# Kernel tuning notes

Measured on AMD Instinct MI355X. Metric: run time of the kernel, lower is better.

The kernel has to match this reference:

```python
import jax, jax.numpy as jnp
import numpy as np


def setup_inputs() -> dict:
    key = jax.random.key(0)
    k1, k2 = jax.random.split(key)
    B, S_ENC, S_DEC, D = 8, 2048, 2048, 1024
    enc_outputs = jax.random.normal(k1, (B, S_ENC, D), dtype=jnp.float32)
    dec_outputs = jax.random.normal(k2, (B, S_DEC, D), dtype=jnp.float32)
    return {"enc_outputs": enc_outputs, "dec_outputs": dec_outputs}


def reference(enc_outputs, dec_outputs):
    # scores: [B, S_enc, S_dec] = enc @ dec^T (unscaled)
    a_t = jnp.einsum('bed,btd->bet', enc_outputs, dec_outputs)
    a_t = jax.nn.softmax(a_t, axis=-1)
    # context: [B, S_dec, D] = a_t^T @ enc
    c_t = jnp.einsum('bet,bed->btd', a_t, enc_outputs)
    return c_t
```

## Files before the change

kernel.cpp:

```cpp
#include <hip/hip_runtime.h>


typedef _Float16 half8 __attribute__((ext_vector_type(8)));
typedef _Float16 half4v __attribute__((ext_vector_type(4)));
typedef float floatx4 __attribute__((ext_vector_type(4)));

__device__ __forceinline__ void async_load16(const _Float16* g, void* l) {
  __builtin_amdgcn_global_load_lds(
      (const __attribute__((address_space(1))) void*)g,
      (__attribute__((address_space(3))) void*)l, 16, 0, 0);
}

template <typename OutT, bool STATS>
__global__ __launch_bounds__(512, 2) void gemm8p(
    const _Float16* __restrict__ A, const _Float16* __restrict__ Bt,
    OutT* __restrict__ C, float2* __restrict__ part_out, int K, long strideA,
    long strideB, long strideC, int ldA, int ldB, int ldC) {
  extern __shared__ char smem_[];
  const int tid = threadIdx.x;
  const int lane = tid & 63;
  const int wave = tid >> 6;
  const int wm = wave >> 2;
  const int wn = wave & 3;
  const int l15 = lane & 15;
  const int lh = lane >> 4;

  const int gx = gridDim.x, gxy = gridDim.x * gridDim.y;
  int fid = blockIdx.z * gxy + blockIdx.y * gx + blockIdx.x;
  const int nwg = gxy * gridDim.z;
  fid = (fid & 7) * (nwg >> 3) + (fid >> 3);
  const int b = fid / gxy;
  const int rem = fid - b * gxy;
  const int m0 = (rem / gx) * 256;
  const int n0 = (rem % gx) * 256;

  A += (long)b * strideA + (long)m0 * ldA;
  Bt += (long)b * strideB + (long)n0 * ldB;
  C += (long)b * strideC;

  const int lb0 = l15 * 128 + ((lh ^ (l15 & 7)) << 4);
  const int lb1 = lb0 ^ 64;
  const char* aBuf[2] = {smem_ + wm * 16384, smem_ + 32768 + wm * 16384};
  const char* bBuf[2] = {
      smem_ + 65536 + (wn >> 1) * 16384 + (wn & 1) * 8192,
      smem_ + 98304 + (wn >> 1) * 16384 + (wn & 1) * 8192};
  char* aSlot[2] = {smem_, smem_ + 32768};
  char* bSlot[2] = {smem_ + 65536, smem_ + 98304};

  const int srow = tid >> 3;
  const int skk = ((tid & 7) ^ (srow & 7)) << 3;
  const _Float16* Ast = A + (long)srow * ldA + skk;
  const _Float16* Bst = Bt + (long)srow * ldB + skk;
  const int dst = tid << 4;

  floatx4 acc[8][4] = {};
  half8 a[4][2], b0[2][2], b1[2][2];

  auto stage = [&](const _Float16* gs, int ld, int k0, char* slot) {
#pragma unroll
    for (int i = 0; i < 4; ++i)
      async_load16(gs + (long)(i * 64) * ld + k0, slot + i * 8192 + dst);
  };
  auto mm = [&](int mh, int nh, half8(&bb)[2][2]) {
    __builtin_amdgcn_s_setprio(1);
#pragma unroll
    for (int s = 0; s < 2; ++s)
#pragma unroll
      for (int q = 0; q < 4; ++q)
#pragma unroll
        for (int n = 0; n < 2; ++n)
          acc[mh * 4 + q][nh * 2 + n] = __builtin_amdgcn_mfma_f32_16x16x32_f16(
              a[q][s], bb[n][s], acc[mh * 4 + q][nh * 2 + n], 0, 0, 0);
    __builtin_amdgcn_s_setprio(0);
  };
  auto bar = [&]() { asm volatile("s_barrier" ::: "memory"); };

  auto quad4 = [&](int cur, int kst, bool last) {
    const char* aB_ = aBuf[cur];
    const char* bB_ = bBuf[cur];
#pragma unroll
    for (int q = 0; q < 4; ++q) {
      a[q][0] = *(const half8*)(aB_ + lb0 + q * 2048);
      a[q][1] = *(const half8*)(aB_ + lb1 + q * 2048);
    }
#pragma unroll
    for (int n = 0; n < 2; ++n) {
      b0[n][0] = *(const half8*)(bB_ + lb0 + n * 2048);
      b0[n][1] = *(const half8*)(bB_ + lb1 + n * 2048);
      b1[n][0] = *(const half8*)(bB_ + lb0 + (n + 2) * 2048);
      b1[n][1] = *(const half8*)(bB_ + lb1 + (n + 2) * 2048);
    }
    bar();
    mm(0, 0, b0);
    bar();
    bar();
    mm(0, 1, b1);
    bar();
#pragma unroll
    for (int q = 0; q < 4; ++q) {
      a[q][0] = *(const half8*)(aB_ + lb0 + (q + 4) * 2048);
      a[q][1] = *(const half8*)(aB_ + lb1 + (q + 4) * 2048);
    }
    if (kst >= 0) stage(Bst, ldB, kst, bSlot[cur]);
    bar();
    mm(1, 1, b1);
    bar();
    if (kst >= 0) stage(Ast, ldA, kst, aSlot[cur]);
    mm(1, 0, b0);
    if (last)
      asm volatile("s_waitcnt vmcnt(0)" ::: "memory");
    else
      asm volatile("s_waitcnt vmcnt(8)" ::: "memory");
    bar();
  };

  stage(Ast, ldA, 0, aSlot[0]);
  stage(Bst, ldB, 0, bSlot[0]);
  stage(Ast, ldA, 64, aSlot[1]);
  stage(Bst, ldB, 64, bSlot[1]);
  asm volatile("s_waitcnt vmcnt(8)" ::: "memory");
  bar();

  const int NT = K >> 6;
  for (int i = 0; i < (NT >> 1) - 1; ++i) {
    quad4(0, (2 * i + 2) * 64, false);
    quad4(1, (2 * i + 3) * 64, false);
  }
  quad4(0, -1, true);
  quad4(1, -1, true);

#pragma unroll
  for (int mf = 0; mf < 8; ++mf) {
    const long r0 = (long)(m0 + wm * 128 + mf * 16 + lh * 4);
#pragma unroll
    for (int nf = 0; nf < 4; ++nf) {
      const int cc = n0 + wn * 64 + nf * 16 + l15;
#pragma unroll
      for (int rr = 0; rr < 4; ++rr)
        C[(r0 + rr) * ldC + cc] = (OutT)acc[mf][nf][rr];
    }
  }

  if constexpr (STATS) {
    float2* sm = (float2*)smem_;
#pragma unroll
    for (int nf = 0; nf < 4; ++nf) {
      float x16[8][4];
#pragma unroll
      for (int mf = 0; mf < 8; ++mf)
#pragma unroll
        for (int rr = 0; rr < 4; ++rr)
          x16[mf][rr] = (float)(_Float16)acc[mf][nf][rr];
      float mx = -1e30f;
#pragma unroll
      for (int mf = 0; mf < 8; ++mf)
#pragma unroll
        for (int rr = 0; rr < 4; ++rr) mx = fmaxf(mx, x16[mf][rr]);
      float ss = 0.f;
#pragma unroll
      for (int mf = 0; mf < 8; ++mf)
#pragma unroll
        for (int rr = 0; rr < 4; ++rr) ss += __expf(x16[mf][rr] - mx);
#pragma unroll
      for (int d = 16; d <= 32; d <<= 1) {
        const float om = __shfl_xor(mx, d, 64);
        const float os = __shfl_xor(ss, d, 64);
        const float m2 = fmaxf(mx, om);
        ss = ss * __expf(mx - m2) + os * __expf(om - m2);
        mx = m2;
      }
      if (lh == 0) sm[wm * 256 + wn * 64 + nf * 16 + l15] = make_float2(mx, ss);
    }
    __syncthreads();
    if (tid < 256) {
      const float2 a0 = sm[tid], a1 = sm[256 + tid];
      const float m2 = fmaxf(a0.x, a1.x);
      const float s2 =
          a0.y * __expf(a0.x - m2) + a1.y * __expf(a1.x - m2);
      part_out[(size_t)(m0 >> 8) * 16384 + (size_t)b * 2048 + n0 + tid] =
          make_float2(m2, s2);
    }
  }
}

__global__ __launch_bounds__(256) void conv_enc(const float* __restrict__ E,
                                                _Float16* __restrict__ Eh,
                                                _Float16* __restrict__ EhT,
                                                int Se, int D) {
  __shared__ _Float16 T[64][72];
  const int b = blockIdx.z;
  const int d0 = blockIdx.x * 64;
  const int e0 = blockIdx.y * 64;
  const float* Eb = E + (size_t)b * Se * D;
  _Float16* Ehb = Eh + (size_t)b * Se * D;
  _Float16* EhTb = EhT + (size_t)b * D * Se;
  const int tid = threadIdx.x;
  const int tx = tid & 15;
  const int ty = tid >> 4;

  half4v h[4];
#pragma unroll
  for (int r = 0; r < 4; ++r) {
    const int e = e0 + ty * 4 + r;
    float4 v = *(const float4*)(Eb + (size_t)e * D + d0 + tx * 4);
    h[r][0] = (_Float16)v.x; h[r][1] = (_Float16)v.y;
    h[r][2] = (_Float16)v.z; h[r][3] = (_Float16)v.w;
    *(half4v*)(Ehb + (size_t)e * D + d0 + tx * 4) = h[r];
  }
#pragma unroll
  for (int c = 0; c < 4; ++c) {
    half4v w;
#pragma unroll
    for (int r = 0; r < 4; ++r) w[r] = h[r][c];
    *(half4v*)&T[tx * 4 + c][ty * 4] = w;
  }
  __syncthreads();
#pragma unroll
  for (int p = 0; p < 2; ++p) {
    const int idx = tid + p * 256;
    const int row = idx >> 3;
    const int ck = idx & 7;
    *(half8*)(EhTb + (size_t)(d0 + row) * Se + e0 + ck * 8) =
        *(const half8*)&T[row][ck * 8];
  }
}

__global__ __launch_bounds__(256) void conv_dec(const float* __restrict__ X,
                                                _Float16* __restrict__ Y) {
  const size_t i = ((size_t)blockIdx.x * 256 + threadIdx.x) * 8;
  float4 a = *(const float4*)(X + i);
  float4 b = *(const float4*)(X + i + 4);
  half8 h;
  h[0] = (_Float16)a.x; h[1] = (_Float16)a.y;
  h[2] = (_Float16)a.z; h[3] = (_Float16)a.w;
  h[4] = (_Float16)b.x; h[5] = (_Float16)b.y;
  h[6] = (_Float16)b.z; h[7] = (_Float16)b.w;
  *(half8*)(Y + i) = h;
}

__global__ __launch_bounds__(256) void stats_combine(
    const float2* __restrict__ part, float* __restrict__ cstat) {
  const int idx = blockIdx.x * 256 + threadIdx.x;
  float2 a = part[idx];
#pragma unroll
  for (int tc = 1; tc < 8; ++tc) {
    const float2 o = part[tc * 16384 + idx];
    const float m2 = fmaxf(a.x, o.x);
    a.y = a.y * __expf(a.x - m2) + o.y * __expf(o.x - m2);
    a.x = m2;
  }
  cstat[idx] = -(a.x * 1.44269504f + log2f(a.y));
}

__global__ __launch_bounds__(256) void norm_stream(
    const _Float16* __restrict__ ST, const float* __restrict__ cstat,
    _Float16* __restrict__ P) {
  const int b = blockIdx.y;
  const int t0 = blockIdx.x * 4;
  const int e = threadIdx.x * 8;
  float c_[8];
  *(float4*)c_ = *(const float4*)(cstat + (size_t)b * 2048 + e);
  *(float4*)(c_ + 4) = *(const float4*)(cstat + (size_t)b * 2048 + e + 4);
  const size_t base = ((size_t)b * 2048 + t0) * 2048 + e;
#pragma unroll
  for (int r = 0; r < 4; ++r) {
    half8 v = *(const half8*)(ST + base + (size_t)r * 2048);
    half8 o;
#pragma unroll
    for (int j = 0; j < 8; ++j)
      o[j] = (_Float16)exp2f((float)v[j] * 1.44269504f + c_[j]);
    *(half8*)(P + base + (size_t)r * 2048) = o;
  }
}

extern "C" void kernel_launch(void* const* d_in, const int* in_sizes, int n_in,
                              void* d_out, int out_size, void* d_ws,
                              size_t ws_size, hipStream_t stream) {
  const float* enc = (const float*)d_in[0];
  const float* dec = (const float*)d_in[1];
  float* out = (float*)d_out;

  const int B = 8, SE = 2048, SD = 2048, D = 1024;
  char* ws = (char*)d_ws;
  _Float16* enc_h = (_Float16*)ws;
  _Float16* dec_h = (_Float16*)(ws + 33554432);
  _Float16* P = (_Float16*)ws;
  _Float16* enc_hT = (_Float16*)(ws + 67108864);
  _Float16* ST = (_Float16*)(ws + 100663296);
  float* cstat = (float*)(ws + 167772160);
  float2* part2 = (float2*)(ws + 167903232);

  static int smem_set = 0;
  if (!smem_set) {
    (void)hipFuncSetAttribute(
        reinterpret_cast<const void*>(&gemm8p<_Float16, true>),
        hipFuncAttributeMaxDynamicSharedMemorySize, 131072);
    (void)hipFuncSetAttribute(
        reinterpret_cast<const void*>(&gemm8p<float, false>),
        hipFuncAttributeMaxDynamicSharedMemorySize, 131072);
    smem_set = 1;
  }

  conv_enc<<<dim3(D / 64, SE / 64, B), 256, 0, stream>>>(enc, enc_h, enc_hT,
                                                         SE, D);
  conv_dec<<<dim3((size_t)B * SD * D / 2048), 256, 0, stream>>>(dec, dec_h);
  gemm8p<_Float16, true><<<dim3(SE / 256, SD / 256, B), 512, 131072, stream>>>(
      dec_h, enc_h, ST, part2, D, (long)SD * D, (long)SE * D, (long)SD * SE,
      D, D, SE);
  stats_combine<<<dim3(64), 256, 0, stream>>>(part2, cstat);
  norm_stream<<<dim3(512, B), 256, 0, stream>>>(ST, cstat, P);
  gemm8p<float, false><<<dim3(D / 256, SD / 256, B), 512, 131072, stream>>>(
      P, enc_hT, out, nullptr, SE, (long)SD * SE, (long)D * SE, (long)SD * D,
      SE, SE, D);
}
```

Baseline: 321.0 us.

## Software-pipeline LDS fragment reads across k-tiles with double-buffered A registers

Restructures the GEMM main loop so the A and B fragments for the next k-tile are read from LDS during the last MFMA block of the current tile, using two A register sets that alternate between iterations. Each quad4 now starts its MFMAs immediately instead of stalling on LDS reads, and the barrier count per quad drops. The cost is higher VGPR pressure from the extra A buffer, which could spill or hurt occupancy under launch_bounds(512,2), and the wait/barrier ordering becomes more delicate.

```diff
diff --git a/kernel.cpp b/kernel.cpp
--- a/kernel.cpp
+++ b/kernel.cpp
@@ -54,14 +54,14 @@
   const int dst = tid << 4;
 
   floatx4 acc[8][4] = {};
-  half8 a[4][2], b0[2][2], b1[2][2];
+  half8 A0[4][2], A1[4][2], b0[2][2], b1[2][2];
 
   auto stage = [&](const _Float16* gs, int ld, int k0, char* slot) {
 #pragma unroll
     for (int i = 0; i < 4; ++i)
       async_load16(gs + (long)(i * 64) * ld + k0, slot + i * 8192 + dst);
   };
-  auto mm = [&](int mh, int nh, half8(&bb)[2][2]) {
+  auto mm = [&](int mh, int nh, half8(&aa)[4][2], half8(&bb)[2][2]) {
     __builtin_amdgcn_s_setprio(1);
 #pragma unroll
     for (int s = 0; s < 2; ++s)
@@ -70,47 +70,48 @@
 #pragma unroll
         for (int n = 0; n < 2; ++n)
           acc[mh * 4 + q][nh * 2 + n] = __builtin_amdgcn_mfma_f32_16x16x32_f16(
-              a[q][s], bb[n][s], acc[mh * 4 + q][nh * 2 + n], 0, 0, 0);
+              aa[q][s], bb[n][s], acc[mh * 4 + q][nh * 2 + n], 0, 0, 0);
     __builtin_amdgcn_s_setprio(0);
   };
   auto bar = [&]() { asm volatile("s_barrier" ::: "memory"); };
-
-  auto quad4 = [&](int cur, int kst, bool last) {
+  auto rdA = [&](half8(&d)[4][2], const char* base, int qo) {
+#pragma unroll
+    for (int q = 0; q < 4; ++q) {
+      d[q][0] = *(const half8*)(base + lb0 + (q + qo) * 2048);
+      d[q][1] = *(const half8*)(base + lb1 + (q + qo) * 2048);
+    }
+  };
+  auto rdB = [&](half8(&d)[2][2], const char* base, int no) {
+#pragma unroll
+    for (int n = 0; n < 2; ++n) {
+      d[n][0] = *(const half8*)(base + lb0 + (n + no) * 2048);
+      d[n][1] = *(const half8*)(base + lb1 + (n + no) * 2048);
+    }
+  };
+
+  auto quad4 = [&](int cur, int kst, bool pf, bool hs, half8(&aC)[4][2],
+                   half8(&aN)[4][2]) {
     const char* aB_ = aBuf[cur];
     const char* bB_ = bBuf[cur];
-#pragma unroll
-    for (int q = 0; q < 4; ++q) {
-      a[q][0] = *(const half8*)(aB_ + lb0 + q * 2048);
-      a[q][1] = *(const half8*)(aB_ + lb1 + q * 2048);
-    }
-#pragma unroll
-    for (int n = 0; n < 2; ++n) {
-      b0[n][0] = *(const half8*)(bB_ + lb0 + n * 2048);
-      b0[n][1] = *(const half8*)(bB_ + lb1 + n * 2048);
-      b1[n][0] = *(const half8*)(bB_ + lb0 + (n + 2) * 2048);
-      b1[n][1] = *(const half8*)(bB_ + lb1 + (n + 2) * 2048);
-    }
+    mm(0, 0, aC, b0);
+    rdB(b1, bB_, 2);
     bar();
-    mm(0, 0, b0);
+    mm(0, 1, aC, b1);
+    rdA(aC, aB_, 4);
+    if (hs) stage(Bst, ldB, kst, bSlot[cur]);
     bar();
+    mm(1, 1, aC, b1);
+    if (hs) stage(Ast, ldA, kst, aSlot[cur]);
+    if (pf) {
+      if (hs)
+        asm volatile("s_waitcnt vmcnt(8)" ::: "memory");
+      else
+        asm volatile("s_waitcnt vmcnt(0)" ::: "memory");
+    }
     bar();
-    mm(0, 1, b1);
-    bar();
-#pragma unroll
-    for (int q = 0; q < 4; ++q) {
-      a[q][0] = *(const half8*)(aB_ + lb0 + (q + 4) * 2048);
-      a[q][1] = *(const half8*)(aB_ + lb1 + (q + 4) * 2048);
-    }
-    if (kst >= 0) stage(Bst, ldB, kst, bSlot[cur]);
-    bar();
-    mm(1, 1, b1);
-    bar();
-    if (kst >= 0) stage(Ast, ldA, kst, aSlot[cur]);
-    mm(1, 0, b0);
-    if (last)
-      asm volatile("s_waitcnt vmcnt(0)" ::: "memory");
-    else
-      asm volatile("s_waitcnt vmcnt(8)" ::: "memory");
+    if (pf) rdA(aN, aBuf[cur ^ 1], 0);
+    mm(1, 0, aC, b0);
+    if (pf) rdB(b0, bBuf[cur ^ 1], 0);
     bar();
   };
 
@@ -120,14 +121,16 @@
   stage(Bst, ldB, 64, bSlot[1]);
   asm volatile("s_waitcnt vmcnt(8)" ::: "memory");
   bar();
+  rdA(A0, aBuf[0], 0);
+  rdB(b0, bBuf[0], 0);
 
   const int NT = K >> 6;
-  for (int i = 0; i < (NT >> 1) - 1; ++i) {
-    quad4(0, (2 * i + 2) * 64, false);
-    quad4(1, (2 * i + 3) * 64, false);
-  }
-  quad4(0, -1, true);
-  quad4(1, -1, true);
+  for (int i = 0; i < NT / 2 - 1; ++i) {
+    quad4(0, (2 * i + 2) * 64, true, true, A0, A1);
+    quad4(1, (2 * i + 3) * 64, true, true, A1, A0);
+  }
+  quad4(0, 0, true, false, A0, A1);
+  quad4(1, 0, false, false, A1, A0);
 
 #pragma unroll
   for (int mf = 0; mf < 8; ++mf) {
```

Measured after the change: 435.8 us. +35.8%, slower.
